# Optimization experiments

Measured on AMD Instinct MI355X. Metric: run time of the kernel, lower is better.

## Reference

```python
import jax, jax.numpy as jnp
import numpy as np

N, M, T, G, D = 1024, 2048, 64, 512, 16
TWO_PI = 6.283185307179586
EPS = 1e-6


def _kernel(dx, dt, alpha, sigma, omega):
    # dx: (..., 2) spatial diff, dt: (...,) temporal diff (assumed >= 0 where used)
    r2 = jnp.sum(dx * dx, axis=-1)
    spatial = jnp.exp(-r2 / (2.0 * sigma * sigma)) / (TWO_PI * sigma * sigma)
    temporal = omega * jnp.exp(-omega * dt)
    return alpha * spatial * temporal


def setup_inputs() -> dict:
    key = jax.random.key(0)
    ks = jax.random.split(key, 8)
    x = jax.random.uniform(ks[0], (N, 2), dtype=jnp.float32)
    t = jnp.sort(jax.random.uniform(ks[1], (N,), dtype=jnp.float32))
    past_x = jax.random.uniform(ks[2], (N, M, 2), dtype=jnp.float32)
    past_t = jax.random.uniform(ks[3], (N, M), dtype=jnp.float32)
    covariates_xt = jax.random.uniform(ks[4], (N, D), dtype=jnp.float32)
    z_grid = jax.random.uniform(ks[5], (T, G, D), dtype=jnp.float32)
    x_grid = jax.random.uniform(ks[6], (G, 2), dtype=jnp.float32)
    t_grid = jnp.arange(T, dtype=jnp.float32) / T  # uniform grid, dt = 1/T
    beta = jax.random.uniform(ks[7], (D,), dtype=jnp.float32)
    return dict(x=x, t=t, past_x=past_x, past_t=past_t,
                covariates_xt=covariates_xt, z_grid=z_grid, x_grid=x_grid,
                t_grid=t_grid, beta=beta,
                alpha=jnp.float32(0.5), sigma=jnp.float32(0.2), omega=jnp.float32(1.0))


def reference(x, t, past_x, past_t, covariates_xt, z_grid, x_grid, t_grid,
              beta, alpha, sigma, omega):
    # ---- log_intensity at events: (N,) ----
    mu = jnp.maximum(covariates_xt @ beta, EPS)                 # baseline, clamp min 1e-6
    t_diff = t[:, None] - past_t                                # (N, M)
    mask = t_diff > 0
    exc = jnp.where(mask,
                    _kernel(x[:, None, :] - past_x,
                            jnp.where(mask, t_diff, 0.0), alpha, sigma, omega),
                    0.0)                                        # (N, M)
    lam = mu + exc.sum(axis=1)
    log_int = jnp.log(lam + EPS)                                # (N,)

    # ---- numerical integral over the (T, G) grid ----
    z_flat = z_grid.reshape(-1, D)                              # (T*G, D)
    x_flat = jnp.tile(x_grid, (T, 1))                           # (T*G, 2)
    t_flat = jnp.repeat(t_grid, G)                              # (T*G,)
    base = jnp.maximum(z_flat @ beta, EPS)                      # (T*G,)
    d_t = t_flat[None, :] - t[:, None]                          # (N, T*G)
    msk = d_t > 0
    nu = jnp.where(msk,
                   _kernel(x_flat[None, :, :] - x[:, None, :],
                           jnp.where(msk, d_t, 0.0), alpha, sigma, omega),
                   0.0)                                         # (N, T*G)
    intensity = base + nu.sum(axis=0)                           # (T*G,)
    dxdy = 1.0 / G
    dt_step = t_grid[1] - t_grid[0]
    integral = intensity.sum() * dxdy * dt_step                 # scalar

    # pack: first N entries = log intensities, last entry = integral
    return jnp.concatenate([log_int, integral[None]])
```

## Files before the change

### kernel.cpp

```cpp
#include <hip/hip_runtime.h>
#include <math.h>

#define N_EV   1024
#define M_PAST 2048
#define T_GRID 64
#define G_GRID 512
#define D_COV  16
#define EPS_F  1e-6f

__global__ void zero_kernel(float* __restrict__ out) {
    out[N_EV] = 0.0f;
}

__global__ __launch_bounds__(256) void base_kernel(
    const float* __restrict__ z_grid,
    const float* __restrict__ beta,
    const float* __restrict__ t_grid,
    float* __restrict__ out) {
    const int tid = threadIdx.x;
    const int row = blockIdx.x * 256 + tid;

    const float4* b4 = (const float4*)beta;
    float4 b0 = b4[0], b1 = b4[1], b2 = b4[2], b3 = b4[3];

    const float4* z4 = (const float4*)(z_grid + (size_t)row * D_COV);
    float4 z0 = z4[0], z1 = z4[1], z2 = z4[2], z3 = z4[3];

    float dot = z0.x*b0.x + z0.y*b0.y + z0.z*b0.z + z0.w*b0.w
              + z1.x*b1.x + z1.y*b1.y + z1.z*b1.z + z1.w*b1.w
              + z2.x*b2.x + z2.y*b2.y + z2.z*b2.z + z2.w*b2.w
              + z3.x*b3.x + z3.y*b3.y + z3.z*b3.z + z3.w*b3.w;
    float v = fmaxf(dot, EPS_F);

    for (int o = 32; o > 0; o >>= 1) v += __shfl_down(v, o, 64);
    __shared__ float sw[4];
    const int lane = tid & 63, wave = tid >> 6;
    if (lane == 0) sw[wave] = v;
    __syncthreads();
    if (tid == 0) {
        float s = sw[0] + sw[1] + sw[2] + sw[3];
        float dt_step = t_grid[1] - t_grid[0];
        float scale = (1.0f / (float)G_GRID) * dt_step;
        atomicAdd(out + N_EV, s * scale);
    }
}

__global__ __launch_bounds__(256) void event_kernel(
    const float* __restrict__ x,
    const float* __restrict__ t,
    const float* __restrict__ past_x,
    const float* __restrict__ past_t,
    const float* __restrict__ cov,
    const float* __restrict__ x_grid,
    const float* __restrict__ t_grid,
    const float* __restrict__ beta,
    const float* __restrict__ alpha_p,
    const float* __restrict__ sigma_p,
    const float* __restrict__ omega_p,
    float* __restrict__ out) {
    const int i   = blockIdx.x;
    const int tid = threadIdx.x;

    const float alpha = alpha_p[0];
    const float sigma = sigma_p[0];
    const float omega = omega_p[0];
    const float inv2s2 = 1.0f / (2.0f * sigma * sigma);
    const float c = alpha * omega / (6.283185307179586f * sigma * sigma);

    const float xi0 = x[2 * i];
    const float xi1 = x[2 * i + 1];
    const float ti  = t[i];

    float excAcc = 0.0f;
    const float4* pt4 = (const float4*)(past_t + (size_t)i * M_PAST);
    const float4* px4 = (const float4*)(past_x + (size_t)i * M_PAST * 2);
    #pragma unroll
    for (int it = 0; it < M_PAST / 1024; ++it) {
        int j4 = it * 256 + tid;
        float4 pt = pt4[j4];
        float4 pa = px4[2 * j4];
        float4 pb = px4[2 * j4 + 1];
        {
            float dt_ = ti - pt.x;
            if (dt_ > 0.0f) {
                float d0 = xi0 - pa.x, d1 = xi1 - pa.y;
                excAcc += __expf(-(d0*d0 + d1*d1) * inv2s2 - omega * dt_);
            }
        }
        {
            float dt_ = ti - pt.y;
            if (dt_ > 0.0f) {
                float d0 = xi0 - pa.z, d1 = xi1 - pa.w;
                excAcc += __expf(-(d0*d0 + d1*d1) * inv2s2 - omega * dt_);
            }
        }
        {
            float dt_ = ti - pt.z;
            if (dt_ > 0.0f) {
                float d0 = xi0 - pb.x, d1 = xi1 - pb.y;
                excAcc += __expf(-(d0*d0 + d1*d1) * inv2s2 - omega * dt_);
            }
        }
        {
            float dt_ = ti - pt.w;
            if (dt_ > 0.0f) {
                float d0 = xi0 - pb.z, d1 = xi1 - pb.w;
                excAcc += __expf(-(d0*d0 + d1*d1) * inv2s2 - omega * dt_);
            }
        }
    }

    float sgAcc = 0.0f;
    {
        const float4* xg4 = (const float4*)x_grid;
        float4 g = xg4[tid];
        float d0 = xi0 - g.x, d1 = xi1 - g.y;
        sgAcc += __expf(-(d0*d0 + d1*d1) * inv2s2);
        d0 = xi0 - g.z; d1 = xi1 - g.w;
        sgAcc += __expf(-(d0*d0 + d1*d1) * inv2s2);
    }

    float ttAcc = 0.0f;
    if (tid < T_GRID) {
        float d = t_grid[tid] - ti;
        if (d > 0.0f) ttAcc = __expf(-omega * d);
    }

    float a1 = excAcc, a2 = sgAcc, a3 = ttAcc;
    for (int o = 32; o > 0; o >>= 1) {
        a1 += __shfl_down(a1, o, 64);
        a2 += __shfl_down(a2, o, 64);
        a3 += __shfl_down(a3, o, 64);
    }
    __shared__ float s1[4], s2[4], s3[4];
    const int lane = tid & 63, wave = tid >> 6;
    if (lane == 0) { s1[wave] = a1; s2[wave] = a2; s3[wave] = a3; }
    __syncthreads();

    if (tid == 0) {
        float exc = s1[0] + s1[1] + s1[2] + s1[3];
        float sg  = s2[0] + s2[1] + s2[2] + s2[3];
        float tt  = s3[0] + s3[1] + s3[2] + s3[3];

        float mu = 0.0f;
        const float* cv = cov + (size_t)i * D_COV;
        #pragma unroll
        for (int k = 0; k < D_COV; ++k) mu += cv[k] * beta[k];
        mu = fmaxf(mu, EPS_F);

        float lam = mu + c * exc;
        out[i] = __logf(lam + EPS_F);

        float dt_step = t_grid[1] - t_grid[0];
        float scale = (1.0f / (float)G_GRID) * dt_step;
        atomicAdd(out + N_EV, c * sg * tt * scale);
    }
}

extern "C" void kernel_launch(void* const* d_in, const int* in_sizes, int n_in,
                              void* d_out, int out_size, void* d_ws, size_t ws_size,
                              hipStream_t stream) {
    const float* x       = (const float*)d_in[0];
    const float* t       = (const float*)d_in[1];
    const float* past_x  = (const float*)d_in[2];
    const float* past_t  = (const float*)d_in[3];
    const float* cov     = (const float*)d_in[4];
    const float* z_grid  = (const float*)d_in[5];
    const float* x_grid  = (const float*)d_in[6];
    const float* t_grid  = (const float*)d_in[7];
    const float* beta    = (const float*)d_in[8];
    const float* alpha_p = (const float*)d_in[9];
    const float* sigma_p = (const float*)d_in[10];
    const float* omega_p = (const float*)d_in[11];
    float* out = (float*)d_out;

    zero_kernel<<<1, 1, 0, stream>>>(out);
    base_kernel<<<(T_GRID * G_GRID) / 256, 256, 0, stream>>>(z_grid, beta, t_grid, out);
    event_kernel<<<N_EV, 256, 0, stream>>>(x, t, past_x, past_t, cov,
                                           x_grid, t_grid, beta,
                                           alpha_p, sigma_p, omega_p, out);
}
```

Measured before the change: 111.9 us.

## Fuse baseline grid computation into event kernel and replace atomics with workspace reduction

Folds the z_grid·beta baseline dot products into the event kernel, with each block handling 32 grid rows, and removes the separate zero and base kernels. Per-block partial integrals go to a workspace buffer instead of an atomicAdd, and a single-block reduce kernel produces the final integral deterministically. The excitation loop is also made branchless by always computing the exp and selecting the result, and the covariate dot product now uses vector loads. This cuts the launch count from three to two and removes atomic contention, at the cost of extra exp work on masked lanes.

```diff
diff --git a/kernel.cpp b/kernel.cpp
--- a/kernel.cpp
+++ b/kernel.cpp
@@ -7,43 +7,7 @@
 #define G_GRID 512
 #define D_COV  16
 #define EPS_F  1e-6f
-
-__global__ void zero_kernel(float* __restrict__ out) {
-    out[N_EV] = 0.0f;
-}
-
-__global__ __launch_bounds__(256) void base_kernel(
-    const float* __restrict__ z_grid,
-    const float* __restrict__ beta,
-    const float* __restrict__ t_grid,
-    float* __restrict__ out) {
-    const int tid = threadIdx.x;
-    const int row = blockIdx.x * 256 + tid;
-
-    const float4* b4 = (const float4*)beta;
-    float4 b0 = b4[0], b1 = b4[1], b2 = b4[2], b3 = b4[3];
-
-    const float4* z4 = (const float4*)(z_grid + (size_t)row * D_COV);
-    float4 z0 = z4[0], z1 = z4[1], z2 = z4[2], z3 = z4[3];
-
-    float dot = z0.x*b0.x + z0.y*b0.y + z0.z*b0.z + z0.w*b0.w
-              + z1.x*b1.x + z1.y*b1.y + z1.z*b1.z + z1.w*b1.w
-              + z2.x*b2.x + z2.y*b2.y + z2.z*b2.z + z2.w*b2.w
-              + z3.x*b3.x + z3.y*b3.y + z3.z*b3.z + z3.w*b3.w;
-    float v = fmaxf(dot, EPS_F);
-
-    for (int o = 32; o > 0; o >>= 1) v += __shfl_down(v, o, 64);
-    __shared__ float sw[4];
-    const int lane = tid & 63, wave = tid >> 6;
-    if (lane == 0) sw[wave] = v;
-    __syncthreads();
-    if (tid == 0) {
-        float s = sw[0] + sw[1] + sw[2] + sw[3];
-        float dt_step = t_grid[1] - t_grid[0];
-        float scale = (1.0f / (float)G_GRID) * dt_step;
-        atomicAdd(out + N_EV, s * scale);
-    }
-}
+#define ROWS_PER_BLOCK 32
 
 __global__ __launch_bounds__(256) void event_kernel(
     const float* __restrict__ x,
@@ -51,13 +15,15 @@
     const float* __restrict__ past_x,
     const float* __restrict__ past_t,
     const float* __restrict__ cov,
+    const float* __restrict__ z_grid,
     const float* __restrict__ x_grid,
     const float* __restrict__ t_grid,
     const float* __restrict__ beta,
     const float* __restrict__ alpha_p,
     const float* __restrict__ sigma_p,
     const float* __restrict__ omega_p,
-    float* __restrict__ out) {
+    float* __restrict__ out,
+    float* __restrict__ ws) {
     const int i   = blockIdx.x;
     const int tid = threadIdx.x;
 
@@ -71,6 +37,9 @@
     const float xi1 = x[2 * i + 1];
     const float ti  = t[i];
 
+    const float4* b4 = (const float4*)beta;
+    const float4 b0 = b4[0], b1 = b4[1], b2 = b4[2], b3 = b4[3];
+
     float excAcc = 0.0f;
     const float4* pt4 = (const float4*)(past_t + (size_t)i * M_PAST);
     const float4* px4 = (const float4*)(past_x + (size_t)i * M_PAST * 2);
@@ -82,31 +51,27 @@
         float4 pb = px4[2 * j4 + 1];
         {
             float dt_ = ti - pt.x;
-            if (dt_ > 0.0f) {
-                float d0 = xi0 - pa.x, d1 = xi1 - pa.y;
-                excAcc += __expf(-(d0*d0 + d1*d1) * inv2s2 - omega * dt_);
-            }
+            float d0 = xi0 - pa.x, d1 = xi1 - pa.y;
+            float e = __expf(-(d0*d0 + d1*d1) * inv2s2 - omega * dt_);
+            excAcc += (dt_ > 0.0f) ? e : 0.0f;
         }
         {
             float dt_ = ti - pt.y;
-            if (dt_ > 0.0f) {
-                float d0 = xi0 - pa.z, d1 = xi1 - pa.w;
-                excAcc += __expf(-(d0*d0 + d1*d1) * inv2s2 - omega * dt_);
-            }
+            float d0 = xi0 - pa.z, d1 = xi1 - pa.w;
+            float e = __expf(-(d0*d0 + d1*d1) * inv2s2 - omega * dt_);
+            excAcc += (dt_ > 0.0f) ? e : 0.0f;
         }
         {
             float dt_ = ti - pt.z;
-            if (dt_ > 0.0f) {
-                float d0 = xi0 - pb.x, d1 = xi1 - pb.y;
-                excAcc += __expf(-(d0*d0 + d1*d1) * inv2s2 - omega * dt_);
-            }
+            float d0 = xi0 - pb.x, d1 = xi1 - pb.y;
+            float e = __expf(-(d0*d0 + d1*d1) * inv2s2 - omega * dt_);
+            excAcc += (dt_ > 0.0f) ? e : 0.0f;
         }
         {
             float dt_ = ti - pt.w;
-            if (dt_ > 0.0f) {
-                float d0 = xi0 - pb.z, d1 = xi1 - pb.w;
-                excAcc += __expf(-(d0*d0 + d1*d1) * inv2s2 - omega * dt_);
-            }
+            float d0 = xi0 - pb.z, d1 = xi1 - pb.w;
+            float e = __expf(-(d0*d0 + d1*d1) * inv2s2 - omega * dt_);
+            excAcc += (dt_ > 0.0f) ? e : 0.0f;
         }
     }
 
@@ -115,7 +80,7 @@
         const float4* xg4 = (const float4*)x_grid;
         float4 g = xg4[tid];
         float d0 = xi0 - g.x, d1 = xi1 - g.y;
-        sgAcc += __expf(-(d0*d0 + d1*d1) * inv2s2);
+        sgAcc  = __expf(-(d0*d0 + d1*d1) * inv2s2);
         d0 = xi0 - g.z; d1 = xi1 - g.w;
         sgAcc += __expf(-(d0*d0 + d1*d1) * inv2s2);
     }
@@ -126,34 +91,66 @@
         if (d > 0.0f) ttAcc = __expf(-omega * d);
     }
 
-    float a1 = excAcc, a2 = sgAcc, a3 = ttAcc;
+    float baseAcc = 0.0f;
+    if (tid < ROWS_PER_BLOCK) {
+        int row = i * ROWS_PER_BLOCK + tid;
+        const float4* z4 = (const float4*)(z_grid + (size_t)row * D_COV);
+        float4 z0 = z4[0], z1 = z4[1], z2 = z4[2], z3 = z4[3];
+        float dot = z0.x*b0.x + z0.y*b0.y + z0.z*b0.z + z0.w*b0.w
+                  + z1.x*b1.x + z1.y*b1.y + z1.z*b1.z + z1.w*b1.w
+                  + z2.x*b2.x + z2.y*b2.y + z2.z*b2.z + z2.w*b2.w
+                  + z3.x*b3.x + z3.y*b3.y + z3.z*b3.z + z3.w*b3.w;
+        baseAcc = fmaxf(dot, EPS_F);
+    }
+
+    float a1 = excAcc, a2 = sgAcc, a3 = ttAcc, a4 = baseAcc;
     for (int o = 32; o > 0; o >>= 1) {
         a1 += __shfl_down(a1, o, 64);
         a2 += __shfl_down(a2, o, 64);
         a3 += __shfl_down(a3, o, 64);
+        a4 += __shfl_down(a4, o, 64);
     }
-    __shared__ float s1[4], s2[4], s3[4];
+    __shared__ float s1[4], s2[4], s3[4], s4[4];
     const int lane = tid & 63, wave = tid >> 6;
-    if (lane == 0) { s1[wave] = a1; s2[wave] = a2; s3[wave] = a3; }
+    if (lane == 0) { s1[wave] = a1; s2[wave] = a2; s3[wave] = a3; s4[wave] = a4; }
     __syncthreads();
 
     if (tid == 0) {
-        float exc = s1[0] + s1[1] + s1[2] + s1[3];
-        float sg  = s2[0] + s2[1] + s2[2] + s2[3];
-        float tt  = s3[0] + s3[1] + s3[2] + s3[3];
+        float exc  = s1[0] + s1[1] + s1[2] + s1[3];
+        float sg   = s2[0] + s2[1] + s2[2] + s2[3];
+        float tt   = s3[0] + s3[1] + s3[2] + s3[3];
+        float base = s4[0] + s4[1] + s4[2] + s4[3];
 
-        float mu = 0.0f;
-        const float* cv = cov + (size_t)i * D_COV;
-        #pragma unroll
-        for (int k = 0; k < D_COV; ++k) mu += cv[k] * beta[k];
+        const float4* cv4 = (const float4*)(cov + (size_t)i * D_COV);
+        float4 c0 = cv4[0], c1 = cv4[1], c2 = cv4[2], c3 = cv4[3];
+        float mu = c0.x*b0.x + c0.y*b0.y + c0.z*b0.z + c0.w*b0.w
+                 + c1.x*b1.x + c1.y*b1.y + c1.z*b1.z + c1.w*b1.w
+                 + c2.x*b2.x + c2.y*b2.y + c2.z*b2.z + c2.w*b2.w
+                 + c3.x*b3.x + c3.y*b3.y + c3.z*b3.z + c3.w*b3.w;
         mu = fmaxf(mu, EPS_F);
 
-        float lam = mu + c * exc;
-        out[i] = __logf(lam + EPS_F);
+        out[i] = __logf(mu + c * exc + EPS_F);
+        ws[i]  = base + c * sg * tt;
+    }
+}
 
+__global__ __launch_bounds__(1024) void reduce_kernel(
+    const float* __restrict__ ws,
+    const float* __restrict__ t_grid,
+    float* __restrict__ out) {
+    const int tid = threadIdx.x;
+    float v = ws[tid];
+    for (int o = 32; o > 0; o >>= 1) v += __shfl_down(v, o, 64);
+    __shared__ float sw[16];
+    const int lane = tid & 63, wave = tid >> 6;
+    if (lane == 0) sw[wave] = v;
+    __syncthreads();
+    if (tid == 0) {
+        float s = 0.0f;
+        #pragma unroll
+        for (int w = 0; w < 16; ++w) s += sw[w];
         float dt_step = t_grid[1] - t_grid[0];
-        float scale = (1.0f / (float)G_GRID) * dt_step;
-        atomicAdd(out + N_EV, c * sg * tt * scale);
+        out[N_EV] = s * (1.0f / (float)G_GRID) * dt_step;
     }
 }
 
@@ -173,10 +170,10 @@
     const float* sigma_p = (const float*)d_in[10];
     const float* omega_p = (const float*)d_in[11];
     float* out = (float*)d_out;
+    float* ws  = (float*)d_ws;
 
-    zero_kernel<<<1, 1, 0, stream>>>(out);
-    base_kernel<<<(T_GRID * G_GRID) / 256, 256, 0, stream>>>(z_grid, beta, t_grid, out);
-    event_kernel<<<N_EV, 256, 0, stream>>>(x, t, past_x, past_t, cov,
+    event_kernel<<<N_EV, 256, 0, stream>>>(x, t, past_x, past_t, cov, z_grid,
                                            x_grid, t_grid, beta,
-                                           alpha_p, sigma_p, omega_p, out);
+                                           alpha_p, sigma_p, omega_p, out, ws);
+    reduce_kernel<<<1, 1024, 0, stream>>>(ws, t_grid, out);
 }
```

Result: faster. 96.05 us (-14.2%).
